# Optimization experiments

Measured on AMD Instinct MI355X. Metric: run time of the kernel, lower is better.

The kernel has to match this reference:

```python
import jax, jax.numpy as jnp
import numpy as np

N_NODES = 50000
N_EDGES = 400000
H, D = 4, 32  # num_heads, per-head dim
NEG_SLOPE = 0.1


def setup_inputs() -> dict:
    key = jax.random.key(0)
    ks = jax.random.split(key, 12)
    inp = {
        'features': jax.random.normal(ks[0], (N_NODES, 256), jnp.float32) * 0.1,
        'src': jax.random.randint(ks[1], (N_EDGES,), 0, N_NODES, jnp.int32),
        'dst': jax.random.randint(ks[2], (N_EDGES,), 0, N_NODES, jnp.int32),
        'w': jax.random.uniform(ks[3], (N_EDGES,), jnp.float32),
        'W1': jax.random.normal(ks[4], (256, 128), jnp.float32) * 0.05,
        'al1': jax.random.normal(ks[5], (H, D), jnp.float32) * 0.1,
        'ar1': jax.random.normal(ks[6], (H, D), jnp.float32) * 0.1,
        'W2': jax.random.normal(ks[7], (128, 128), jnp.float32) * 0.05,
        'al2': jax.random.normal(ks[8], (H, D), jnp.float32) * 0.1,
        'ar2': jax.random.normal(ks[9], (H, D), jnp.float32) * 0.1,
        'Wout': jax.random.normal(ks[10], (256, 128), jnp.float32) * 0.05,
        'bout': jnp.zeros((128,), jnp.float32),
    }
    return inp


def _gat_layer(x, W, al, ar, src, dst, w):
    # x: [N, in_dim] -> ft: [N, H, D]
    ft = (x @ W).reshape(-1, H, D)
    el = jnp.einsum('nhd,hd->nh', ft, al)  # left attention logits per node
    er = jnp.einsum('nhd,hd->nh', ft, ar)
    # edge logits: leaky_relu(el[src] + er[dst]), then edge-weight scaling
    e = jax.nn.leaky_relu(el[src] + er[dst], negative_slope=NEG_SLOPE)  # [E, H]
    e = w[:, None] * e
    # segment softmax over incoming edges of each destination node
    m = jax.ops.segment_max(e, dst, num_segments=N_NODES)  # [N, H]
    a = jnp.exp(e - m[dst])
    s = jax.ops.segment_sum(a, dst, num_segments=N_NODES)
    a = a / s[dst]  # [E, H]
    # weighted scatter-sum aggregation: rst[dst] += a * ft[src]
    msg = ft[src] * a[:, :, None]  # [E, H, D]
    rst = jax.ops.segment_sum(msg, dst, num_segments=N_NODES)  # [N, H, D]
    # activation=relu, then concat heads (contiguous -> reshape)
    return jax.nn.relu(rst).reshape(-1, H * D)


def reference(features, src, dst, w, W1, al1, ar1, W2, al2, ar2, Wout, bout):
    x1 = _gat_layer(features, W1, al1, ar1, src, dst, w)  # [N, 128]
    x2 = _gat_layer(x1, W2, al2, ar2, src, dst, w)        # [N, 128]
    h = jnp.concatenate([x1, x2], axis=-1)                # [N, 256]
    return h @ Wout + bout                                # [N, 128]
```

## Files before the change

kernel.cpp:

```cpp
#include <hip/hip_runtime.h>
#include <math.h>

#define NEG_SLOPE 0.1f
#define MAXDEG 64

typedef unsigned short u16;
typedef unsigned int u32;
typedef _Float16 f16;
typedef f16 f16x2 __attribute__((ext_vector_type(2)));
typedef f16 f16x8 __attribute__((ext_vector_type(8)));
typedef float f32x4 __attribute__((ext_vector_type(4)));

#define GLLDS16(g, l) __builtin_amdgcn_global_load_lds( \
    (const __attribute__((address_space(1))) void*)(g), \
    (__attribute__((address_space(3))) void*)(l), 16, 0, 0)


__device__ __forceinline__ void cast_panel(const float* __restrict__ W,
                                           const float* __restrict__ al,
                                           const float* __restrict__ ar,
                                           u16* __restrict__ bp, int t, int NC) {
    int per_kt = NC * 16;
    int kt = t / per_kt;
    int rem = t - kt * per_kt;
    int nt = rem >> 8;
    int w32 = rem & 255;
    int kg = w32 >> 6;
    int col = (w32 >> 2) & 15;
    int kp = (w32 & 3) * 2;
    int n = nt * 16 + col;
    int k = kt * 32 + kg * 8 + kp;
    float v0 = 0.f, v1 = 0.f;
    if (n < 128) {
        v0 = W[(size_t)k * 128 + n];
        v1 = W[(size_t)(k + 1) * 128 + n];
    } else if (n < 136) {
        const float* av = (n < 132) ? al : ar;
        int h = (n < 132) ? (n - 128) : (n - 132);
        float s0 = 0.f, s1 = 0.f;
        for (int d = 0; d < 32; d++) {
            float a = av[h * 32 + d];
            s0 += W[(size_t)k * 128 + h * 32 + d] * a;
            s1 += W[(size_t)(k + 1) * 128 + h * 32 + d] * a;
        }
        v0 = s0; v1 = s1;
    }
    f16x2 p;
    p.x = (f16)v0; p.y = (f16)v1;
    *(f16x2*)&((u32*)bp)[t] = p;
}

__global__ void cast_k(const float* __restrict__ W1, const float* __restrict__ al1,
                       const float* __restrict__ ar1, u16* __restrict__ b1,
                       const float* __restrict__ W2, const float* __restrict__ al2,
                       const float* __restrict__ ar2, u16* __restrict__ b2,
                       const float* __restrict__ W3, u16* __restrict__ b3,
                       int* __restrict__ fill, int N) {
    int t = blockIdx.x * 256 + threadIdx.x;
    if (t < N) fill[t] = 0;
    if (t < 18432) cast_panel(W1, al1, ar1, b1, t, 144);
    else if (t < 27648) cast_panel(W2, al2, ar2, b2, t - 18432, 144);
    else if (t < 44032) cast_panel(W3, nullptr, nullptr, b3, t - 27648, 128);
}


template <int NT>
__device__ __forceinline__ void gemm_tile(
        const void* __restrict__ Av, int a_is_f16, int lda,
        const u16* __restrict__ Bp,
        const float* __restrict__ bias, float* __restrict__ Cf,
        u16* __restrict__ Ch, float* __restrict__ el, float* __restrict__ er,
        int M, int K, int tile, char* shmem) {
    u16* As = (u16*)shmem;
    u16* Bs = (u16*)(shmem + 16384);
    int tid = threadIdx.x;
    int wv = tid >> 6, lane = tid & 63;
    int mrow = lane & 15;
    int row0 = tile * 128;

    f32x4 acc[NT];
#pragma unroll
    for (int nt = 0; nt < NT; nt++) acc[nt] = (f32x4){0.f, 0.f, 0.f, 0.f};

    for (int k0 = 0; k0 < K; k0 += 64) {
        int kt0 = k0 >> 5;
        const u16* Bsrc = Bp + (size_t)kt0 * (NT * 512);
#pragma unroll
        for (int i = 0; i < (2 * NT * 64 + 511) / 512; i++) {
            int c = tid + i * 512;
            if (c < 2 * NT * 64) GLLDS16(Bsrc + (size_t)c * 8, &Bs[c * 8]);
        }
#pragma unroll
        for (int i = 0; i < 2; i++) {
            int c = tid + i * 512;
            int slice = c >> 9, w32 = c & 511;
            int rblk = w32 >> 6, kg = (w32 >> 4) & 3, rr = w32 & 15;
            int row = row0 + rblk * 16 + rr;
            int k = k0 + slice * 32 + kg * 8;
            if (a_is_f16) {
                const u16* Ah = (const u16*)Av;
                GLLDS16(Ah + (size_t)row * lda + k, &As[c * 8]);
            } else {
                const float* Af = (const float*)Av;
                if (row > M - 1) row = M - 1;
                const float* ap = &Af[(size_t)row * lda + k];
                float4 v0 = *(const float4*)ap;
                float4 v1 = *(const float4*)(ap + 4);
                f16x8 pk;
                pk[0] = (f16)v0.x; pk[1] = (f16)v0.y; pk[2] = (f16)v0.z; pk[3] = (f16)v0.w;
                pk[4] = (f16)v1.x; pk[5] = (f16)v1.y; pk[6] = (f16)v1.z; pk[7] = (f16)v1.w;
                *(f16x8*)&As[c * 8] = pk;
            }
        }
        __syncthreads();
#pragma unroll
        for (int kk = 0; kk < 2; kk++) {
            f16x8 ah = *(const f16x8*)&As[kk * 4096 + wv * 512 + lane * 8];
#pragma unroll
            for (int nt = 0; nt < NT; nt++) {
                f16x8 bh = *(const f16x8*)&Bs[kk * (NT * 512) + nt * 512 + lane * 8];
                acc[nt] = __builtin_amdgcn_mfma_f32_16x16x32_f16(ah, bh, acc[nt], 0, 0, 0);
            }
        }
        __syncthreads();
    }

    int rbase = row0 + wv * 16 + (lane >> 4) * 4;
#pragma unroll
    for (int nt = 0; nt < 8; nt++) {
        int col = nt * 16 + mrow;
        float bv = bias ? bias[col] : 0.f;
        f32x4 v = acc[nt];
#pragma unroll
        for (int reg = 0; reg < 4; reg++) {
            int rr = rbase + reg;
            if (rr < M) {
                float val = v[reg] + bv;
                if (Cf) Cf[(size_t)rr * 128 + col] = val;
                if (Ch) *(f16*)&Ch[(size_t)rr * 128 + col] = (f16)val;
            }
        }
    }
    if (NT == 9) {
        f32x4 v = acc[8];
#pragma unroll
        for (int reg = 0; reg < 4; reg++) {
            int rr = rbase + reg;
            if (rr < M) {
                if (mrow < 4) el[rr * 4 + mrow] = v[reg];
                else if (mrow < 8) er[rr * 4 + (mrow - 4)] = v[reg];
            }
        }
    }
}

template <int NT>
__global__ __launch_bounds__(512, 6) void gemm_k(
        const void* __restrict__ Av, int a_is_f16, int lda,
        const u16* __restrict__ Bp, const float* __restrict__ bias,
        float* __restrict__ Cf, u16* __restrict__ Ch,
        float* __restrict__ el, float* __restrict__ er, int M, int K) {
    alignas(16) __shared__ char sh[16384 + NT * 2048];
    gemm_tile<NT>(Av, a_is_f16, lda, Bp, bias, Cf, Ch, el, er, M, K, blockIdx.x, sh);
}

__global__ __launch_bounds__(512, 6) void g1s_k(
        const float* __restrict__ features, const u16* __restrict__ b1,
        u16* __restrict__ fth, float* __restrict__ el, float* __restrict__ er,
        int M, int gb,
        const int* __restrict__ src, const int* __restrict__ dst,
        const float* __restrict__ w,
        int* __restrict__ fill, int2* __restrict__ edge_s, int E) {
    alignas(16) __shared__ char sh[16384 + 9 * 2048];
    if ((int)blockIdx.x < gb) {
        gemm_tile<9>(features, 0, 256, b1, nullptr, nullptr, fth, el, er,
                     M, 256, blockIdx.x, sh);
    } else {
        int e = (blockIdx.x - gb) * 512 + threadIdx.x;
        if (e < E) {
            int d = dst[e];
            int pos = atomicAdd(&fill[d], 1);
            if (pos < MAXDEG)
                edge_s[(size_t)d * MAXDEG + pos] = make_int2(src[e], __float_as_int(w[e]));
        }
    }
}


__device__ __forceinline__ float lrelu(float x) {
    return x > 0.f ? x : NEG_SLOPE * x;
}

__global__ __launch_bounds__(256) void agg_k(const u32* __restrict__ fth2,
                                             const float4* __restrict__ el4,
                                             const float4* __restrict__ er4,
                                             const int2* __restrict__ edge_s,
                                             const int* __restrict__ fill,
                                             u16* __restrict__ xcat,
                                             int ooff, int N, int ngroups) {
    __shared__ float4 sA[256];
    __shared__ int sS[256];
    int wv = threadIdx.x >> 6;
    int lane = threadIdx.x & 63;
    int head = lane >> 4;
    for (int g = blockIdx.x; g < ngroups; g += gridDim.x) {
        int n = g * 4 + wv;
        if (n >= N) continue;
        int deg = fill[n];
        if (deg > MAXDEG) deg = MAXDEG;
        u16* op = &xcat[(size_t)n * 256 + ooff + 2 * lane];
        if (deg == 0) {
            *(u32*)op = 0;
            continue;
        }
        float4 ern = er4[n];
        float acc0 = 0.f, acc1 = 0.f;
        float4 a = make_float4(0.f, 0.f, 0.f, 0.f);
        int s = 0;
        if (lane < deg) {
            int2 ep = edge_s[(size_t)n * MAXDEG + lane];
            s = ep.x;
            float we = __int_as_float(ep.y);
            float4 e = el4[s];
            a.x = __expf(we * lrelu(e.x + ern.x));
            a.y = __expf(we * lrelu(e.y + ern.y));
            a.z = __expf(we * lrelu(e.z + ern.z));
            a.w = __expf(we * lrelu(e.w + ern.w));
        }
        float4 sm = a;
        for (int m = 1; m < deg; m <<= 1) {
            sm.x += __shfl_xor(sm.x, m);
            sm.y += __shfl_xor(sm.y, m);
            sm.z += __shfl_xor(sm.z, m);
            sm.w += __shfl_xor(sm.w, m);
        }
        a.x *= __builtin_amdgcn_rcpf(sm.x);
        a.y *= __builtin_amdgcn_rcpf(sm.y);
        a.z *= __builtin_amdgcn_rcpf(sm.z);
        a.w *= __builtin_amdgcn_rcpf(sm.w);
        sA[wv * 64 + lane] = a;
        sS[wv * 64 + lane] = s;
        const float* sAf = (const float*)&sA[wv * 64];
        const int* sSp = &sS[wv * 64];
        int i = 0;
        for (; i + 8 <= deg; i += 8) {
            float wg[8];
            u32 pp[8];
#pragma unroll
            for (int j = 0; j < 8; j++) {
                wg[j] = sAf[(i + j) * 4 + head];
                u32 su = __builtin_amdgcn_readfirstlane((u32)sSp[i + j]);
                pp[j] = fth2[(size_t)su * 64 + lane];
            }
#pragma unroll
            for (int j = 0; j < 8; j++) {
                f16x2 hp = *(const f16x2*)&pp[j];
                acc0 += wg[j] * (float)hp.x;
                acc1 += wg[j] * (float)hp.y;
            }
        }
        for (; i < deg; i++) {
            float wgt = sAf[i * 4 + head];
            u32 su = __builtin_amdgcn_readfirstlane((u32)sSp[i]);
            u32 p = fth2[(size_t)su * 64 + lane];
            f16x2 hp = *(const f16x2*)&p;
            acc0 += wgt * (float)hp.x;
            acc1 += wgt * (float)hp.y;
        }
        f16x2 hv;
        hv.x = (f16)fmaxf(acc0, 0.f);
        hv.y = (f16)fmaxf(acc1, 0.f);
        *(f16x2*)op = hv;
    }
}


extern "C" void kernel_launch(void* const* d_in, const int* in_sizes, int n_in,
                              void* d_out, int out_size, void* d_ws, size_t ws_size,
                              hipStream_t stream) {
    const float* features = (const float*)d_in[0];
    const int* src = (const int*)d_in[1];
    const int* dst = (const int*)d_in[2];
    const float* w = (const float*)d_in[3];
    const float* W1 = (const float*)d_in[4];
    const float* al1 = (const float*)d_in[5];
    const float* ar1 = (const float*)d_in[6];
    const float* W2 = (const float*)d_in[7];
    const float* al2 = (const float*)d_in[8];
    const float* ar2 = (const float*)d_in[9];
    const float* Wout = (const float*)d_in[10];
    const float* bout = (const float*)d_in[11];
    float* out = (float*)d_out;

    int N = in_sizes[0] / 256;
    int E = in_sizes[1];
    int Mpad = ((N + 127) / 128) * 128;

    char* ws = (char*)d_ws;
    size_t off = 0;
    auto alloc = [&](size_t bytes) -> void* {
        void* p = ws + off;
        off = (off + bytes + 255) & ~(size_t)255;
        return p;
    };
    size_t Nr = ((size_t)N * 4 + 255) & ~(size_t)255;
    int* fill = (int*)alloc(Nr);
    int2* edge_s = (int2*)alloc((size_t)N * MAXDEG * 8);
    u16* fth = (u16*)alloc((size_t)Mpad * 128 * 2);
    float* el = (float*)alloc((size_t)N * 4 * 4);
    float* er = (float*)alloc((size_t)N * 4 * 4);
    u16* xcat = (u16*)alloc((size_t)Mpad * 256 * 2);
    u16* b1 = (u16*)alloc((size_t)18432 * 4);
    u16* b2 = (u16*)alloc((size_t)9216 * 4);
    u16* b3 = (u16*)alloc((size_t)16384 * 4);
    (void)ws_size; (void)n_in; (void)out_size;

    int eb = (E + 511) / 512;
    int ng = (N + 3) / 4;
    int ab = ng < 2048 ? ng : 2048;
    int gb = Mpad / 128;
    int cb = (N + 255) / 256;

    cast_k<<<cb, 256, 0, stream>>>(W1, al1, ar1, b1, W2, al2, ar2, b2, Wout, b3,
                                   fill, N);

    g1s_k<<<gb + eb, 512, 0, stream>>>(features, b1, fth, el, er, N, gb,
                                       src, dst, w, fill, edge_s, E);
    agg_k<<<ab, 256, 0, stream>>>((const u32*)fth, (const float4*)el, (const float4*)er,
                                  edge_s, fill, xcat, 0, N, ng);

    gemm_k<9><<<gb, 512, 0, stream>>>(xcat, 1, 256, b2, nullptr,
                                      nullptr, fth, el, er, N, 128);
    agg_k<<<ab, 256, 0, stream>>>((const u32*)fth, (const float4*)el, (const float4*)er,
                                  edge_s, fill, xcat, 128, N, ng);

    gemm_k<8><<<gb, 512, 0, stream>>>(xcat, 1, 256, b3, bout,
                                      out, nullptr, nullptr, nullptr, N, 256);
}
```

Before: 219.5 us.

## Software-pipeline per-node metadata and el loads across grid-stride iterations in agg_k

The aggregation kernel now prefetches fill, edge_s, and er4 two grid-stride iterations ahead, and el4 one iteration ahead. This hides the chain of dependent loads (degree, then edge source, then el of the source) behind the current node's gather work. In exchange it uses more registers, issues loads for all 64 lanes even when the degree is smaller, and clamps source indices so reads of unused slots stay in bounds.

```diff
diff --git a/kernel.cpp b/kernel.cpp
--- a/kernel.cpp
+++ b/kernel.cpp
@@ -203,75 +203,106 @@
     int wv = threadIdx.x >> 6;
     int lane = threadIdx.x & 63;
     int head = lane >> 4;
-    for (int g = blockIdx.x; g < ngroups; g += gridDim.x) {
-        int n = g * 4 + wv;
-        if (n >= N) continue;
-        int deg = fill[n];
-        if (deg > MAXDEG) deg = MAXDEG;
-        u16* op = &xcat[(size_t)n * 256 + ooff + 2 * lane];
-        if (deg == 0) {
+    int stride = gridDim.x;
+
+#define LDA(gg, v_, n_, dg_, ep_, ern_)                         \
+    {                                                           \
+        int nn = (gg) * 4 + wv;                                 \
+        v_ = ((gg) < ngroups) && (nn < N);                      \
+        n_ = v_ ? nn : 0;                                       \
+        dg_ = fill[n_];                                         \
+        ep_ = edge_s[(size_t)n_ * MAXDEG + lane];               \
+        ern_ = er4[n_];                                         \
+    }
+
+    int g = blockIdx.x;
+    if (g >= ngroups) return;
+
+    bool vC; int nC, dgC; int2 epC; float4 ernC;
+    LDA(g, vC, nC, dgC, epC, ernC);
+    int sC = epC.x;
+    sC = sC < 0 ? 0 : (sC > N - 1 ? N - 1 : sC);
+    float4 eC = el4[sC];
+
+    bool vN; int nN, dgN; int2 epN; float4 ernN;
+    LDA(g + stride, vN, nN, dgN, epN, ernN);
+
+    for (; g < ngroups; g += stride) {
+        bool vN2; int nN2, dgN2; int2 epN2; float4 ernN2;
+        LDA(g + 2 * stride, vN2, nN2, dgN2, epN2, ernN2);
+
+        int deg = vC ? (dgC > MAXDEG ? MAXDEG : dgC) : 0;
+        u16* op = &xcat[(size_t)nC * 256 + ooff + 2 * lane];
+
+        float4 a = make_float4(0.f, 0.f, 0.f, 0.f);
+        if (deg > 0) {
+            if (lane < deg) {
+                float we = __int_as_float(epC.y);
+                a.x = __expf(we * lrelu(eC.x + ernC.x));
+                a.y = __expf(we * lrelu(eC.y + ernC.y));
+                a.z = __expf(we * lrelu(eC.z + ernC.z));
+                a.w = __expf(we * lrelu(eC.w + ernC.w));
+            }
+            float4 sm = a;
+            for (int m = 1; m < deg; m <<= 1) {
+                sm.x += __shfl_xor(sm.x, m);
+                sm.y += __shfl_xor(sm.y, m);
+                sm.z += __shfl_xor(sm.z, m);
+                sm.w += __shfl_xor(sm.w, m);
+            }
+            a.x *= __builtin_amdgcn_rcpf(sm.x);
+            a.y *= __builtin_amdgcn_rcpf(sm.y);
+            a.z *= __builtin_amdgcn_rcpf(sm.z);
+            a.w *= __builtin_amdgcn_rcpf(sm.w);
+            sA[wv * 64 + lane] = a;
+            sS[wv * 64 + lane] = (lane < deg) ? epC.x : 0;
+        }
+
+        int sN = epN.x;
+        sN = sN < 0 ? 0 : (sN > N - 1 ? N - 1 : sN);
+        float4 eN = el4[sN];
+
+        if (deg > 0) {
+            float acc0 = 0.f, acc1 = 0.f;
+            const float* sAf = (const float*)&sA[wv * 64];
+            const int* sSp = &sS[wv * 64];
+            int i = 0;
+            for (; i + 8 <= deg; i += 8) {
+                float wg[8];
+                u32 pp[8];
+#pragma unroll
+                for (int j = 0; j < 8; j++) {
+                    wg[j] = sAf[(i + j) * 4 + head];
+                    u32 su = __builtin_amdgcn_readfirstlane((u32)sSp[i + j]);
+                    pp[j] = fth2[(size_t)su * 64 + lane];
+                }
+#pragma unroll
+                for (int j = 0; j < 8; j++) {
+                    f16x2 hp = *(const f16x2*)&pp[j];
+                    acc0 += wg[j] * (float)hp.x;
+                    acc1 += wg[j] * (float)hp.y;
+                }
+            }
+            for (; i < deg; i++) {
+                float wgt = sAf[i * 4 + head];
+                u32 su = __builtin_amdgcn_readfirstlane((u32)sSp[i]);
+                u32 p = fth2[(size_t)su * 64 + lane];
+                f16x2 hp = *(const f16x2*)&p;
+                acc0 += wgt * (float)hp.x;
+                acc1 += wgt * (float)hp.y;
+            }
+            f16x2 hv;
+            hv.x = (f16)fmaxf(acc0, 0.f);
+            hv.y = (f16)fmaxf(acc1, 0.f);
+            *(f16x2*)op = hv;
+        } else if (vC) {
             *(u32*)op = 0;
-            continue;
-        }
-        float4 ern = er4[n];
-        float acc0 = 0.f, acc1 = 0.f;
-        float4 a = make_float4(0.f, 0.f, 0.f, 0.f);
-        int s = 0;
-        if (lane < deg) {
-            int2 ep = edge_s[(size_t)n * MAXDEG + lane];
-            s = ep.x;
-            float we = __int_as_float(ep.y);
-            float4 e = el4[s];
-            a.x = __expf(we * lrelu(e.x + ern.x));
-            a.y = __expf(we * lrelu(e.y + ern.y));
-            a.z = __expf(we * lrelu(e.z + ern.z));
-            a.w = __expf(we * lrelu(e.w + ern.w));
-        }
-        float4 sm = a;
-        for (int m = 1; m < deg; m <<= 1) {
-            sm.x += __shfl_xor(sm.x, m);
-            sm.y += __shfl_xor(sm.y, m);
-            sm.z += __shfl_xor(sm.z, m);
-            sm.w += __shfl_xor(sm.w, m);
-        }
-        a.x *= __builtin_amdgcn_rcpf(sm.x);
-        a.y *= __builtin_amdgcn_rcpf(sm.y);
-        a.z *= __builtin_amdgcn_rcpf(sm.z);
-        a.w *= __builtin_amdgcn_rcpf(sm.w);
-        sA[wv * 64 + lane] = a;
-        sS[wv * 64 + lane] = s;
-        const float* sAf = (const float*)&sA[wv * 64];
-        const int* sSp = &sS[wv * 64];
-        int i = 0;
-        for (; i + 8 <= deg; i += 8) {
-            float wg[8];
-            u32 pp[8];
-#pragma unroll
-            for (int j = 0; j < 8; j++) {
-                wg[j] = sAf[(i + j) * 4 + head];
-                u32 su = __builtin_amdgcn_readfirstlane((u32)sSp[i + j]);
-                pp[j] = fth2[(size_t)su * 64 + lane];
-            }
-#pragma unroll
-            for (int j = 0; j < 8; j++) {
-                f16x2 hp = *(const f16x2*)&pp[j];
-                acc0 += wg[j] * (float)hp.x;
-                acc1 += wg[j] * (float)hp.y;
-            }
-        }
-        for (; i < deg; i++) {
-            float wgt = sAf[i * 4 + head];
-            u32 su = __builtin_amdgcn_readfirstlane((u32)sSp[i]);
-            u32 p = fth2[(size_t)su * 64 + lane];
-            f16x2 hp = *(const f16x2*)&p;
-            acc0 += wgt * (float)hp.x;
-            acc1 += wgt * (float)hp.y;
-        }
-        f16x2 hv;
-        hv.x = (f16)fmaxf(acc0, 0.f);
-        hv.y = (f16)fmaxf(acc1, 0.f);
-        *(f16x2*)op = hv;
-    }
+        }
+
+        vC = vN; nC = nN; dgC = dgN; epC = epN; ernC = ernN; eC = eN;
+        vN = vN2; nN = nN2; dgN = dgN2; epN = epN2; ernN = ernN2;
+    }
+#undef LDA
 }
 
 
```

New measurement: 220.0 us. No clear change (+0.2%).
